# Kernel tuning notes

Measured on AMD Instinct MI355X. Metric: run time of the kernel, lower is better.

The kernel has to match this reference:

```python
import jax, jax.numpy as jnp
import numpy as np

B, T, D = 1, 4096, 1024
H = 16
HEAD_DIM = D // H
WINDOW = 256


def setup_inputs() -> dict:
    key = jax.random.key(0)
    k1, k2, k3 = jax.random.split(key, 3)
    x = jax.random.normal(k1, (B, T, D), dtype=jnp.float32)
    # torch nn.Linear(D, 3D) weight is (3D, D); we store transposed (D, 3D) for x @ W
    w_qkv = jax.random.normal(k2, (D, 3 * D), dtype=jnp.float32) * (1.0 / np.sqrt(D))
    w_out = jax.random.normal(k3, (D, D), dtype=jnp.float32) * (1.0 / np.sqrt(D))
    return {"x": x, "w_qkv": w_qkv, "w_out": w_out}


def reference(x, w_qkv, w_out):
    b, t, d = x.shape
    qkv = x @ w_qkv                                   # (B, T, 3D)
    q, k, v = jnp.split(qkv, 3, axis=-1)
    def split_heads(a):                               # (B, T, D) -> (B, H, T, dh)
        return a.reshape(b, t, H, HEAD_DIM).transpose(0, 2, 1, 3)
    q, k, v = split_heads(q), split_heads(k), split_heads(v)
    scale = jnp.sqrt(jnp.float32(HEAD_DIM))
    scores = jnp.einsum('bhqd,bhkd->bhqk', q, k) / scale   # (B, H, T, T)
    rows = jnp.arange(t)[:, None]
    cols = jnp.arange(t)[None, :]
    # causal sliding window: j <= i and j >= i - window + 1
    mask = (cols <= rows) & (cols >= rows - WINDOW + 1)     # (T, T) bool
    scores = jnp.where(mask[None, None], scores, -jnp.inf)
    attn = jax.nn.softmax(scores, axis=-1)
    out = jnp.einsum('bhqk,bhkd->bhqd', attn, v)            # (B, H, T, dh)
    out = out.transpose(0, 2, 1, 3).reshape(b, t, d)        # merge heads
    return out @ w_out
```

## Files before the change

### kernel.cpp

```cpp
#include <hip/hip_runtime.h>
#include <hip/hip_bf16.h>

#define T_SEQ 4096
#define DMODEL 1024
#define NH 16
#define DH 64
#define N_QKV 3072

typedef __attribute__((ext_vector_type(8))) short bf16x8;
typedef __attribute__((ext_vector_type(4))) float f32x4;

__device__ inline void gload_lds16(const __hip_bfloat16* g, __hip_bfloat16* l) {
  __builtin_amdgcn_global_load_lds(
      (const __attribute__((address_space(1))) void*)g,
      (__attribute__((address_space(3))) void*)l, 16, 0, 0);
}

__global__ void cast_x_kernel(const float* __restrict__ in,
                              __hip_bfloat16* __restrict__ out, int n) {
  int i = (blockIdx.x * 256 + threadIdx.x) * 4;
  if (i >= n) return;
  float4 v = *(const float4*)(in + i);
  ushort4 o;
  o.x = __bfloat16_as_ushort(__float2bfloat16(v.x));
  o.y = __bfloat16_as_ushort(__float2bfloat16(v.y));
  o.z = __bfloat16_as_ushort(__float2bfloat16(v.z));
  o.w = __bfloat16_as_ushort(__float2bfloat16(v.w));
  *(ushort4*)((unsigned short*)out + i) = o;
}

__global__ void transpose_cast_kernel(const float* __restrict__ in,
                                      __hip_bfloat16* __restrict__ out,
                                      int NN, int KK) {
  __shared__ float tile[32][33];
  int bn = blockIdx.x * 32, bk = blockIdx.y * 32;
  int tx = threadIdx.x & 31, ty = threadIdx.x >> 5;
#pragma unroll
  for (int r = 0; r < 32; r += 8)
    tile[ty + r][tx] = in[(size_t)(bk + ty + r) * NN + bn + tx];
  __syncthreads();
#pragma unroll
  for (int r = 0; r < 32; r += 8)
    out[(size_t)(bn + ty + r) * KK + bk + tx] = __float2bfloat16(tile[tx][ty + r]);
}

__global__ void transpose_v_kernel(const __hip_bfloat16* __restrict__ qkv,
                                   __hip_bfloat16* __restrict__ vt) {
  __shared__ unsigned short tile[32][33];
  int c0 = blockIdx.x * 32;
  int t0 = blockIdx.y * 32;
  int tx = threadIdx.x & 31, ty = threadIdx.x >> 5;
  const unsigned short* in = (const unsigned short*)qkv;
  unsigned short* out = (unsigned short*)vt;
#pragma unroll
  for (int r = 0; r < 32; r += 8)
    tile[ty + r][tx] = in[(size_t)(t0 + ty + r) * N_QKV + 2 * DMODEL + c0 + tx];
  __syncthreads();
#pragma unroll
  for (int r = 0; r < 32; r += 8)
    out[(size_t)(c0 + ty + r) * T_SEQ + t0 + tx] = tile[tx][ty + r];
}

__global__ __launch_bounds__(512, 2) void gemm8_qkv(
    const __hip_bfloat16* __restrict__ A, const __hip_bfloat16* __restrict__ Bt,
    __hip_bfloat16* __restrict__ C) {
  const int K = DMODEL;
  const int N = N_QKV;
  __shared__ alignas(16) __hip_bfloat16 Ab[3][256 * 64];
  __shared__ alignas(16) __hip_bfloat16 Bb[2][192 * 64];

  const int tid = threadIdx.x;
  const int lane = tid & 63;
  const int w = tid >> 6;
  const int wr = w >> 2, wc = w & 3;
  const int frow = lane & 15, fgrp = lane >> 4;

  const int bid = blockIdx.x;
  const int sbid = (bid & 7) * 32 + (bid >> 3);
  const int mb = sbid >> 4, nb = sbid & 15;
  const int brow = mb << 8, bcol = nb * 192;

  const int srow = lane >> 3;
  const int sslot = (lane & 7) ^ srow;
  const __hip_bfloat16* aSrcA = A + (size_t)(brow + w * 32 + srow) * K + sslot * 8;
  const __hip_bfloat16* aSrcB = Bt + (size_t)(bcol + w * 24 + srow) * K + sslot * 8;
  const int dstA = (w * 32 + srow) * 64 + (lane & 7) * 8;
  const int dstB = (w * 24 + srow) * 64 + (lane & 7) * 8;

  f32x4 acc[8][3] = {};

#pragma unroll
  for (int i = 0; i < 4; i++)
    gload_lds16(aSrcA + (size_t)(i * 8) * K, &Ab[0][dstA + i * 8 * 64]);
#pragma unroll
  for (int i = 0; i < 3; i++)
    gload_lds16(aSrcB + (size_t)(i * 8) * K, &Bb[0][dstB + i * 8 * 64]);
#pragma unroll
  for (int i = 0; i < 4; i++)
    gload_lds16(aSrcA + (size_t)(i * 8) * K + 64, &Ab[1][dstA + i * 8 * 64]);

  for (int t = 0; t < 16; ++t) {
    if (t < 15)
      asm volatile("s_waitcnt vmcnt(4)" ::: "memory");
    else
      asm volatile("s_waitcnt vmcnt(0)" ::: "memory");
    __builtin_amdgcn_s_barrier();

    const __hip_bfloat16* As = &Ab[t % 3][0];
    const __hip_bfloat16* Bs = &Bb[t & 1][0];
    bf16x8 bfrag[3][2], afrag[4][2];

#pragma unroll
    for (int n = 0; n < 3; n++) {
      int row = wc * 48 + n * 16 + frow;
#pragma unroll
      for (int kh = 0; kh < 2; kh++) {
        int slot = (kh * 4 + fgrp) ^ (row & 7);
        bfrag[n][kh] = *(const bf16x8*)(Bs + row * 64 + slot * 8);
      }
    }
#pragma unroll
    for (int m = 0; m < 4; m++) {
      int row = wr * 128 + m * 16 + frow;
#pragma unroll
      for (int kh = 0; kh < 2; kh++) {
        int slot = (kh * 4 + fgrp) ^ (row & 7);
        afrag[m][kh] = *(const bf16x8*)(As + row * 64 + slot * 8);
      }
    }
    if (t + 1 < 16) {
      __hip_bfloat16* bd = &Bb[(t + 1) & 1][0];
#pragma unroll
      for (int i = 0; i < 3; i++)
        gload_lds16(aSrcB + (size_t)(i * 8) * K + (t + 1) * 64, bd + dstB + i * 8 * 64);
    }
    __builtin_amdgcn_s_barrier();
    __builtin_amdgcn_s_setprio(1);
#pragma unroll
    for (int m = 0; m < 4; m++)
#pragma unroll
      for (int n = 0; n < 3; n++) {
        acc[m][n] = __builtin_amdgcn_mfma_f32_16x16x32_bf16(afrag[m][0], bfrag[n][0], acc[m][n], 0, 0, 0);
        acc[m][n] = __builtin_amdgcn_mfma_f32_16x16x32_bf16(afrag[m][1], bfrag[n][1], acc[m][n], 0, 0, 0);
      }
    __builtin_amdgcn_s_setprio(0);
    __builtin_amdgcn_s_barrier();

#pragma unroll
    for (int m = 0; m < 4; m++) {
      int row = wr * 128 + (m + 4) * 16 + frow;
#pragma unroll
      for (int kh = 0; kh < 2; kh++) {
        int slot = (kh * 4 + fgrp) ^ (row & 7);
        afrag[m][kh] = *(const bf16x8*)(As + row * 64 + slot * 8);
      }
    }
    if (t + 2 < 16) {
      __hip_bfloat16* ad = &Ab[(t + 2) % 3][0];
#pragma unroll
      for (int i = 0; i < 4; i++)
        gload_lds16(aSrcA + (size_t)(i * 8) * K + (t + 2) * 64, ad + dstA + i * 8 * 64);
    }
    __builtin_amdgcn_s_barrier();
    __builtin_amdgcn_s_setprio(1);
#pragma unroll
    for (int m = 0; m < 4; m++)
#pragma unroll
      for (int n = 0; n < 3; n++) {
        acc[m + 4][n] = __builtin_amdgcn_mfma_f32_16x16x32_bf16(afrag[m][0], bfrag[n][0], acc[m + 4][n], 0, 0, 0);
        acc[m + 4][n] = __builtin_amdgcn_mfma_f32_16x16x32_bf16(afrag[m][1], bfrag[n][1], acc[m + 4][n], 0, 0, 0);
      }
    __builtin_amdgcn_s_setprio(0);
  }

  const int orow0 = brow + wr * 128 + 4 * fgrp;
  const int ocol0 = bcol + wc * 48 + frow;
#pragma unroll
  for (int m = 0; m < 8; m++)
#pragma unroll
    for (int n = 0; n < 3; n++) {
      int col = ocol0 + n * 16;
      float sc = (col < DMODEL) ? 0.125f : 1.0f;
#pragma unroll
      for (int j = 0; j < 4; j++) {
        int row = orow0 + m * 16 + j;
        C[(size_t)row * N + col] = __float2bfloat16(acc[m][n][j] * sc);
      }
    }
}

__global__ __launch_bounds__(256) void gemm_out(
    const __hip_bfloat16* __restrict__ A, const __hip_bfloat16* __restrict__ Bt,
    float* __restrict__ C) {
  const int K = DMODEL, N = DMODEL;
  __shared__ alignas(16) __hip_bfloat16 Ab[4][128 * 32];
  __shared__ alignas(16) __hip_bfloat16 Bb[4][64 * 32];
  const int tid = threadIdx.x, lane = tid & 63, w = tid >> 6;
  const int wr = w >> 1, wc = w & 1;
  const int frow = lane & 15, fgrp = lane >> 4;
  const int bid = blockIdx.x;
  const int sbid = (bid & 7) * 64 + (bid >> 3);
  const int mb = sbid >> 4, nb = sbid & 15;
  const int brow = mb * 128, bcol = nb * 64;

  const int rrA = w * 32 + (lane >> 2);
  const int swzA = ((lane & 3) ^ ((rrA >> 1) & 3)) << 3;
  const int rrB = w * 16 + (lane >> 2);
  const int swzB = ((lane & 3) ^ ((rrB >> 1) & 3)) << 3;
  const __hip_bfloat16* aA0 = A + (size_t)(brow + rrA) * K + swzA;
  const __hip_bfloat16* aB0 = Bt + (size_t)(bcol + rrB) * K + swzB;
  const int dA0 = (w * 32) * 32, dA1 = (w * 32 + 16) * 32, dB0 = (w * 16) * 32;

  f32x4 acc[4][2] = {};
#pragma unroll
  for (int t = 0; t < 3; t++) {
    gload_lds16(aA0 + t * 32, &Ab[t][dA0]);
    gload_lds16(aA0 + 16 * (size_t)K + t * 32, &Ab[t][dA1]);
    gload_lds16(aB0 + t * 32, &Bb[t][dB0]);
  }
  for (int g = 0; g < 32; ++g) {
    if (g <= 29)
      asm volatile("s_waitcnt vmcnt(6)" ::: "memory");
    else if (g == 30)
      asm volatile("s_waitcnt vmcnt(3)" ::: "memory");
    else
      asm volatile("s_waitcnt vmcnt(0)" ::: "memory");
    __builtin_amdgcn_s_barrier();
    const __hip_bfloat16* As = Ab[g & 3];
    const __hip_bfloat16* Bs = Bb[g & 3];
    bf16x8 af[4], bfr[2];
#pragma unroll
    for (int m = 0; m < 4; m++) {
      int row = wr * 64 + m * 16 + frow;
      af[m] = *(const bf16x8*)(As + row * 32 + ((fgrp ^ ((row >> 1) & 3)) << 3));
    }
#pragma unroll
    for (int n = 0; n < 2; n++) {
      int row = wc * 32 + n * 16 + frow;
      bfr[n] = *(const bf16x8*)(Bs + row * 32 + ((fgrp ^ ((row >> 1) & 3)) << 3));
    }
    if (g <= 28) {
      int t = g + 3;
      gload_lds16(aA0 + t * 32, &Ab[t & 3][dA0]);
      gload_lds16(aA0 + 16 * (size_t)K + t * 32, &Ab[t & 3][dA1]);
      gload_lds16(aB0 + t * 32, &Bb[t & 3][dB0]);
    }
    __builtin_amdgcn_s_barrier();
    __builtin_amdgcn_s_setprio(1);
#pragma unroll
    for (int m = 0; m < 4; m++)
#pragma unroll
      for (int n = 0; n < 2; n++)
        acc[m][n] = __builtin_amdgcn_mfma_f32_16x16x32_bf16(af[m], bfr[n], acc[m][n], 0, 0, 0);
    __builtin_amdgcn_s_setprio(0);
  }
  const int orow0 = brow + wr * 64 + 4 * fgrp;
  const int ocol0 = bcol + wc * 32 + frow;
#pragma unroll
  for (int m = 0; m < 4; m++)
#pragma unroll
    for (int n = 0; n < 2; n++)
#pragma unroll
      for (int j = 0; j < 4; j++)
        C[(size_t)(orow0 + m * 16 + j) * N + ocol0 + n * 16] = acc[m][n][j];
}

__global__ __launch_bounds__(256) void swa_kernel(
    const __hip_bfloat16* __restrict__ qkv, const __hip_bfloat16* __restrict__ vt,
    __hip_bfloat16* __restrict__ attn_out) {
  const int b = blockIdx.x;
  const int s = (b & 7) * 128 + (b >> 3);
  const int h = s >> 6;
  const int qb = s & 63;
  const int tid = threadIdx.x;
  const int lane = tid & 63;
  const int w = tid >> 6;
  const int frow = lane & 15;
  const int fgrp = lane >> 4;
  const int fk = fgrp * 8;

  __shared__ alignas(16) __hip_bfloat16 Ks[2][64 * 64];
  __shared__ alignas(16) __hip_bfloat16 Vs[2][64 * 64];
  __shared__ alignas(16) __hip_bfloat16 Pl[4][16 * 72];

  const int qrow_g = qb * 64 + w * 16 + frow;
  bf16x8 aq[2];
  {
    const __hip_bfloat16* qptr = qkv + (size_t)qrow_g * N_QKV + h * DH;
    aq[0] = *(const bf16x8*)(qptr + fk);
    aq[1] = *(const bf16x8*)(qptr + 32 + fk);
  }

  f32x4 o[4] = {};
  float l_run[4] = {0.f, 0.f, 0.f, 0.f};

  const int srow = lane >> 3;
  const int ssw = (((lane & 7) ^ srow) << 3);
  const __hip_bfloat16* kbase =
      qkv + (size_t)(w * 16 + srow) * N_QKV + DMODEL + h * DH + ssw;
  const __hip_bfloat16* vbase =
      vt + (size_t)(h * DH + w * 16 + srow) * T_SEQ + ssw;

  const int kb0 = qb >= 4 ? qb - 4 : 0;

  {
    const __hip_bfloat16* ks = kbase + (size_t)kb0 * 64 * N_QKV;
    gload_lds16(ks, &Ks[0][w * 16 * 64]);
    gload_lds16(ks + 8 * (size_t)N_QKV, &Ks[0][(w * 16 + 8) * 64]);
    const __hip_bfloat16* vs = vbase + kb0 * 64;
    gload_lds16(vs, &Vs[0][w * 16 * 64]);
    gload_lds16(vs + 8 * (size_t)T_SEQ, &Vs[0][(w * 16 + 8) * 64]);
  }

  for (int kb = kb0; kb <= qb; kb++) {
    const int buf = (kb - kb0) & 1;
    if (kb < qb) {
      const __hip_bfloat16* ks = kbase + (size_t)(kb + 1) * 64 * N_QKV;
      gload_lds16(ks, &Ks[buf ^ 1][w * 16 * 64]);
      gload_lds16(ks + 8 * (size_t)N_QKV, &Ks[buf ^ 1][(w * 16 + 8) * 64]);
      const __hip_bfloat16* vs = vbase + (kb + 1) * 64;
      gload_lds16(vs, &Vs[buf ^ 1][w * 16 * 64]);
      gload_lds16(vs + 8 * (size_t)T_SEQ, &Vs[buf ^ 1][(w * 16 + 8) * 64]);
      asm volatile("s_waitcnt vmcnt(4)" ::: "memory");
    } else {
      asm volatile("s_waitcnt vmcnt(0)" ::: "memory");
    }
    __builtin_amdgcn_s_barrier();

    f32x4 sc[4];
#pragma unroll
    for (int n = 0; n < 4; n++) sc[n] = (f32x4){0.f, 0.f, 0.f, 0.f};
#pragma unroll
    for (int n = 0; n < 4; n++) {
      int rowk = n * 16 + frow;
      int x = rowk & 7;
      bf16x8 bk0 = *(const bf16x8*)(&Ks[buf][rowk * 64 + ((fgrp ^ x) << 3)]);
      bf16x8 bk1 = *(const bf16x8*)(&Ks[buf][rowk * 64 + (((4 + fgrp) ^ x) << 3)]);
      sc[n] = __builtin_amdgcn_mfma_f32_16x16x32_bf16(aq[0], bk0, sc[n], 0, 0, 0);
      sc[n] = __builtin_amdgcn_mfma_f32_16x16x32_bf16(aq[1], bk1, sc[n], 0, 0, 0);
    }

    const bool edge_hi = (kb == qb);
    const bool edge_lo = (kb == qb - 4);
#pragma unroll
    for (int r = 0; r < 4; r++) {
      const int row_l = w * 16 + 4 * fgrp + r;
      float rs = 0.f;
#pragma unroll
      for (int n = 0; n < 4; n++) {
        int col_l = n * 16 + frow;
        bool valid = (!edge_hi || col_l <= row_l) && (!edge_lo || col_l > row_l);
        float p = valid ? __expf(sc[n][r]) : 0.f;
        sc[n][r] = p;
        rs += p;
      }
      l_run[r] += rs;
    }

    __hip_bfloat16* pw = &Pl[w][0];
#pragma unroll
    for (int n = 0; n < 4; n++)
#pragma unroll
      for (int r = 0; r < 4; r++)
        pw[(4 * fgrp + r) * 72 + n * 16 + frow] = __float2bfloat16(sc[n][r]);

#pragma unroll
    for (int c = 0; c < 2; c++) {
      bf16x8 ap = *(const bf16x8*)(pw + frow * 72 + c * 32 + fk);
#pragma unroll
      for (int nd = 0; nd < 4; nd++) {
        int rowd = nd * 16 + frow;
        int x = rowd & 7;
        bf16x8 bv = *(const bf16x8*)(&Vs[buf][rowd * 64 + (((c * 4 + fgrp) ^ x) << 3)]);
        o[nd] = __builtin_amdgcn_mfma_f32_16x16x32_bf16(ap, bv, o[nd], 0, 0, 0);
      }
    }
    __builtin_amdgcn_s_barrier();
  }

#pragma unroll
  for (int r = 0; r < 4; r++) {
    float l = l_run[r];
    l += __shfl_xor(l, 1);
    l += __shfl_xor(l, 2);
    l += __shfl_xor(l, 4);
    l += __shfl_xor(l, 8);
    l_run[r] = l;
  }
#pragma unroll
  for (int nd = 0; nd < 4; nd++)
#pragma unroll
    for (int r = 0; r < 4; r++) {
      float v = o[nd][r] / l_run[r];
      attn_out[(size_t)(qb * 64 + w * 16 + 4 * fgrp + r) * DMODEL + h * DH + nd * 16 + frow] =
          __float2bfloat16(v);
    }
}

extern "C" void kernel_launch(void* const* d_in, const int* in_sizes, int n_in,
                              void* d_out, int out_size, void* d_ws, size_t ws_size,
                              hipStream_t stream) {
  const float* x = (const float*)d_in[0];
  const float* w_qkv = (const float*)d_in[1];
  const float* w_out = (const float*)d_in[2];
  float* out = (float*)d_out;

  char* ws = (char*)d_ws;
  __hip_bfloat16* x_bf = (__hip_bfloat16*)ws;
  __hip_bfloat16* vt = (__hip_bfloat16*)ws;
  __hip_bfloat16* wqkvT = (__hip_bfloat16*)(ws + 8388608);
  __hip_bfloat16* woutT = (__hip_bfloat16*)(ws + 14680064);
  __hip_bfloat16* qkv_bf = (__hip_bfloat16*)(ws + 16777216);
  __hip_bfloat16* attn_bf = (__hip_bfloat16*)(ws + 41943040);

  cast_x_kernel<<<4096, 256, 0, stream>>>(x, x_bf, T_SEQ * DMODEL);
  transpose_cast_kernel<<<dim3(N_QKV / 32, DMODEL / 32), 256, 0, stream>>>(w_qkv, wqkvT, N_QKV, DMODEL);
  transpose_cast_kernel<<<dim3(DMODEL / 32, DMODEL / 32), 256, 0, stream>>>(w_out, woutT, DMODEL, DMODEL);

  gemm8_qkv<<<(T_SEQ / 256) * (N_QKV / 192), 512, 0, stream>>>(x_bf, wqkvT, qkv_bf);

  transpose_v_kernel<<<dim3(DMODEL / 32, T_SEQ / 32), 256, 0, stream>>>(qkv_bf, vt);

  swa_kernel<<<(T_SEQ / 64) * NH, 256, 0, stream>>>(qkv_bf, vt, attn_bf);

  gemm_out<<<512, 256, 0, stream>>>(attn_bf, woutT, out);
}
```

Baseline: 85.82 us.

## Fuse prep kernels, split QKV GEMM k-halves, enlarge output GEMM tile

Folds the x cast and both weight transpose-casts into one launch indexed by block id, removing two kernel launches. Restructures the QKV GEMM inner loop into four phases, one per 32-wide k half and A half, with smaller fragment sets and the next tile's global-to-LDS loads split across the phases. This is meant to cut register pressure and spread memory traffic. The output GEMM moves from 128x64 to 128x128 tiles with half the blocks, for more operand reuse at the cost of fewer blocks in flight and more LDS per block.

```diff
diff --git a/kernel.cpp b/kernel.cpp
--- a/kernel.cpp
+++ b/kernel.cpp
@@ -16,24 +16,37 @@
       (__attribute__((address_space(3))) void*)l, 16, 0, 0);
 }
 
-__global__ void cast_x_kernel(const float* __restrict__ in,
-                              __hip_bfloat16* __restrict__ out, int n) {
-  int i = (blockIdx.x * 256 + threadIdx.x) * 4;
-  if (i >= n) return;
-  float4 v = *(const float4*)(in + i);
-  ushort4 o;
-  o.x = __bfloat16_as_ushort(__float2bfloat16(v.x));
-  o.y = __bfloat16_as_ushort(__float2bfloat16(v.y));
-  o.z = __bfloat16_as_ushort(__float2bfloat16(v.z));
-  o.w = __bfloat16_as_ushort(__float2bfloat16(v.w));
-  *(ushort4*)((unsigned short*)out + i) = o;
-}
-
-__global__ void transpose_cast_kernel(const float* __restrict__ in,
-                                      __hip_bfloat16* __restrict__ out,
-                                      int NN, int KK) {
+__global__ void prep_kernel(const float* __restrict__ x,
+                            const float* __restrict__ w_qkv,
+                            const float* __restrict__ w_out,
+                            __hip_bfloat16* __restrict__ x_bf,
+                            __hip_bfloat16* __restrict__ wqkvT,
+                            __hip_bfloat16* __restrict__ woutT) {
   __shared__ float tile[32][33];
-  int bn = blockIdx.x * 32, bk = blockIdx.y * 32;
+  const int b = blockIdx.x;
+  if (b < 4096) {
+    int i = (b * 256 + threadIdx.x) * 4;
+    float4 v = *(const float4*)(x + i);
+    ushort4 o;
+    o.x = __bfloat16_as_ushort(__float2bfloat16(v.x));
+    o.y = __bfloat16_as_ushort(__float2bfloat16(v.y));
+    o.z = __bfloat16_as_ushort(__float2bfloat16(v.z));
+    o.w = __bfloat16_as_ushort(__float2bfloat16(v.w));
+    *(ushort4*)((unsigned short*)x_bf + i) = o;
+    return;
+  }
+  const float* in;
+  __hip_bfloat16* out;
+  int NN, KK, bn, bk;
+  if (b < 7168) {
+    int idx = b - 4096;
+    in = w_qkv; out = wqkvT; NN = N_QKV; KK = DMODEL;
+    bn = (idx % 96) * 32; bk = (idx / 96) * 32;
+  } else {
+    int idx = b - 7168;
+    in = w_out; out = woutT; NN = DMODEL; KK = DMODEL;
+    bn = (idx % 32) * 32; bk = (idx / 32) * 32;
+  }
   int tx = threadIdx.x & 31, ty = threadIdx.x >> 5;
 #pragma unroll
   for (int r = 0; r < 32; r += 8)
@@ -108,68 +121,93 @@
 
     const __hip_bfloat16* As = &Ab[t % 3][0];
     const __hip_bfloat16* Bs = &Bb[t & 1][0];
-    bf16x8 bfrag[3][2], afrag[4][2];
-
+    bf16x8 bfrag[3], af[4];
+
+    if (t + 1 < 16) {
+      __hip_bfloat16* bd = &Bb[(t + 1) & 1][0];
+#pragma unroll
+      for (int i = 0; i < 3; i++)
+        gload_lds16(aSrcB + (size_t)(i * 8) * K + (t + 1) * 64, bd + dstB + i * 8 * 64);
+    }
 #pragma unroll
     for (int n = 0; n < 3; n++) {
       int row = wc * 48 + n * 16 + frow;
-#pragma unroll
-      for (int kh = 0; kh < 2; kh++) {
-        int slot = (kh * 4 + fgrp) ^ (row & 7);
-        bfrag[n][kh] = *(const bf16x8*)(Bs + row * 64 + slot * 8);
-      }
+      bfrag[n] = *(const bf16x8*)(Bs + row * 64 + (fgrp ^ (row & 7)) * 8);
     }
 #pragma unroll
     for (int m = 0; m < 4; m++) {
       int row = wr * 128 + m * 16 + frow;
-#pragma unroll
-      for (int kh = 0; kh < 2; kh++) {
-        int slot = (kh * 4 + fgrp) ^ (row & 7);
-        afrag[m][kh] = *(const bf16x8*)(As + row * 64 + slot * 8);
-      }
-    }
-    if (t + 1 < 16) {
-      __hip_bfloat16* bd = &Bb[(t + 1) & 1][0];
-#pragma unroll
-      for (int i = 0; i < 3; i++)
-        gload_lds16(aSrcB + (size_t)(i * 8) * K + (t + 1) * 64, bd + dstB + i * 8 * 64);
+      af[m] = *(const bf16x8*)(As + row * 64 + (fgrp ^ (row & 7)) * 8);
     }
     __builtin_amdgcn_s_barrier();
     __builtin_amdgcn_s_setprio(1);
 #pragma unroll
     for (int m = 0; m < 4; m++)
 #pragma unroll
-      for (int n = 0; n < 3; n++) {
-        acc[m][n] = __builtin_amdgcn_mfma_f32_16x16x32_bf16(afrag[m][0], bfrag[n][0], acc[m][n], 0, 0, 0);
-        acc[m][n] = __builtin_amdgcn_mfma_f32_16x16x32_bf16(afrag[m][1], bfrag[n][1], acc[m][n], 0, 0, 0);
-      }
+      for (int n = 0; n < 3; n++)
+        acc[m][n] = __builtin_amdgcn_mfma_f32_16x16x32_bf16(af[m], bfrag[n], acc[m][n], 0, 0, 0);
     __builtin_amdgcn_s_setprio(0);
     __builtin_amdgcn_s_barrier();
 
+    if (t + 2 < 16) {
+      __hip_bfloat16* ad = &Ab[(t + 2) % 3][0];
+#pragma unroll
+      for (int i = 0; i < 2; i++)
+        gload_lds16(aSrcA + (size_t)(i * 8) * K + (t + 2) * 64, ad + dstA + i * 8 * 64);
+    }
 #pragma unroll
     for (int m = 0; m < 4; m++) {
       int row = wr * 128 + (m + 4) * 16 + frow;
-#pragma unroll
-      for (int kh = 0; kh < 2; kh++) {
-        int slot = (kh * 4 + fgrp) ^ (row & 7);
-        afrag[m][kh] = *(const bf16x8*)(As + row * 64 + slot * 8);
-      }
-    }
+      af[m] = *(const bf16x8*)(As + row * 64 + (fgrp ^ (row & 7)) * 8);
+    }
+    __builtin_amdgcn_s_barrier();
+    __builtin_amdgcn_s_setprio(1);
+#pragma unroll
+    for (int m = 0; m < 4; m++)
+#pragma unroll
+      for (int n = 0; n < 3; n++)
+        acc[m + 4][n] = __builtin_amdgcn_mfma_f32_16x16x32_bf16(af[m], bfrag[n], acc[m + 4][n], 0, 0, 0);
+    __builtin_amdgcn_s_setprio(0);
+    __builtin_amdgcn_s_barrier();
+
     if (t + 2 < 16) {
       __hip_bfloat16* ad = &Ab[(t + 2) % 3][0];
 #pragma unroll
-      for (int i = 0; i < 4; i++)
+      for (int i = 2; i < 4; i++)
         gload_lds16(aSrcA + (size_t)(i * 8) * K + (t + 2) * 64, ad + dstA + i * 8 * 64);
     }
+#pragma unroll
+    for (int n = 0; n < 3; n++) {
+      int row = wc * 48 + n * 16 + frow;
+      bfrag[n] = *(const bf16x8*)(Bs + row * 64 + ((4 + fgrp) ^ (row & 7)) * 8);
+    }
+#pragma unroll
+    for (int m = 0; m < 4; m++) {
+      int row = wr * 128 + m * 16 + frow;
+      af[m] = *(const bf16x8*)(As + row * 64 + ((4 + fgrp) ^ (row & 7)) * 8);
+    }
     __builtin_amdgcn_s_barrier();
     __builtin_amdgcn_s_setprio(1);
 #pragma unroll
     for (int m = 0; m < 4; m++)
 #pragma unroll
-      for (int n = 0; n < 3; n++) {
-        acc[m + 4][n] = __builtin_amdgcn_mfma_f32_16x16x32_bf16(afrag[m][0], bfrag[n][0], acc[m + 4][n], 0, 0, 0);
-        acc[m + 4][n] = __builtin_amdgcn_mfma_f32_16x16x32_bf16(afrag[m][1], bfrag[n][1], acc[m + 4][n], 0, 0, 0);
-      }
+      for (int n = 0; n < 3; n++)
+        acc[m][n] = __builtin_amdgcn_mfma_f32_16x16x32_bf16(af[m], bfrag[n], acc[m][n], 0, 0, 0);
+    __builtin_amdgcn_s_setprio(0);
+    __builtin_amdgcn_s_barrier();
+
+#pragma unroll
+    for (int m = 0; m < 4; m++) {
+      int row = wr * 128 + (m + 4) * 16 + frow;
+      af[m] = *(const bf16x8*)(As + row * 64 + ((4 + fgrp) ^ (row & 7)) * 8);
+    }
+    __builtin_amdgcn_s_barrier();
+    __builtin_amdgcn_s_setprio(1);
+#pragma unroll
+    for (int m = 0; m < 4; m++)
+#pragma unroll
+      for (int n = 0; n < 3; n++)
+        acc[m + 4][n] = __builtin_amdgcn_mfma_f32_16x16x32_bf16(af[m], bfrag[n], acc[m + 4][n], 0, 0, 0);
     __builtin_amdgcn_s_setprio(0);
   }
 
@@ -194,72 +232,72 @@
     float* __restrict__ C) {
   const int K = DMODEL, N = DMODEL;
   __shared__ alignas(16) __hip_bfloat16 Ab[4][128 * 32];
-  __shared__ alignas(16) __hip_bfloat16 Bb[4][64 * 32];
+  __shared__ alignas(16) __hip_bfloat16 Bb[4][128 * 32];
   const int tid = threadIdx.x, lane = tid & 63, w = tid >> 6;
   const int wr = w >> 1, wc = w & 1;
   const int frow = lane & 15, fgrp = lane >> 4;
   const int bid = blockIdx.x;
-  const int sbid = (bid & 7) * 64 + (bid >> 3);
-  const int mb = sbid >> 4, nb = sbid & 15;
-  const int brow = mb * 128, bcol = nb * 64;
-
-  const int rrA = w * 32 + (lane >> 2);
-  const int swzA = ((lane & 3) ^ ((rrA >> 1) & 3)) << 3;
-  const int rrB = w * 16 + (lane >> 2);
-  const int swzB = ((lane & 3) ^ ((rrB >> 1) & 3)) << 3;
-  const __hip_bfloat16* aA0 = A + (size_t)(brow + rrA) * K + swzA;
-  const __hip_bfloat16* aB0 = Bt + (size_t)(bcol + rrB) * K + swzB;
-  const int dA0 = (w * 32) * 32, dA1 = (w * 32 + 16) * 32, dB0 = (w * 16) * 32;
-
-  f32x4 acc[4][2] = {};
+  const int sbid = (bid & 7) * 32 + (bid >> 3);
+  const int mb = sbid >> 3, nb = sbid & 7;
+  const int brow = mb * 128, bcol = nb * 128;
+
+  const int sr = tid >> 2;
+  const int swz = ((tid & 3) ^ ((sr >> 1) & 3)) << 3;
+  const __hip_bfloat16* aA = A + (size_t)(brow + sr) * K + swz;
+  const __hip_bfloat16* aB = Bt + (size_t)(bcol + sr) * K + swz;
+  const int dlo = sr * 32 + (tid & 3) * 8;
+  const int dhi = (sr + 64) * 32 + (tid & 3) * 8;
+
+  f32x4 acc[4][4] = {};
 #pragma unroll
   for (int t = 0; t < 3; t++) {
-    gload_lds16(aA0 + t * 32, &Ab[t][dA0]);
-    gload_lds16(aA0 + 16 * (size_t)K + t * 32, &Ab[t][dA1]);
-    gload_lds16(aB0 + t * 32, &Bb[t][dB0]);
-  }
-  for (int g = 0; g < 32; ++g) {
-    if (g <= 29)
-      asm volatile("s_waitcnt vmcnt(6)" ::: "memory");
-    else if (g == 30)
-      asm volatile("s_waitcnt vmcnt(3)" ::: "memory");
+    gload_lds16(aA + t * 32, &Ab[t][dlo]);
+    gload_lds16(aA + 64 * (size_t)K + t * 32, &Ab[t][dhi]);
+    gload_lds16(aB + t * 32, &Bb[t][dlo]);
+    gload_lds16(aB + 64 * (size_t)K + t * 32, &Bb[t][dhi]);
+  }
+  for (int t = 0; t < 32; ++t) {
+    if (t < 30)
+      asm volatile("s_waitcnt vmcnt(8)" ::: "memory");
+    else if (t == 30)
+      asm volatile("s_waitcnt vmcnt(4)" ::: "memory");
     else
       asm volatile("s_waitcnt vmcnt(0)" ::: "memory");
     __builtin_amdgcn_s_barrier();
-    const __hip_bfloat16* As = Ab[g & 3];
-    const __hip_bfloat16* Bs = Bb[g & 3];
-    bf16x8 af[4], bfr[2];
+    const __hip_bfloat16* As = Ab[t & 3];
+    const __hip_bfloat16* Bs = Bb[t & 3];
+    if (t + 3 < 32) {
+      gload_lds16(aA + (t + 3) * 32, &Ab[(t + 3) & 3][dlo]);
+      gload_lds16(aA + 64 * (size_t)K + (t + 3) * 32, &Ab[(t + 3) & 3][dhi]);
+      gload_lds16(aB + (t + 3) * 32, &Bb[(t + 3) & 3][dlo]);
+      gload_lds16(aB + 64 * (size_t)K + (t + 3) * 32, &Bb[(t + 3) & 3][dhi]);
+    }
+    bf16x8 af[4], bfr[4];
 #pragma unroll
     for (int m = 0; m < 4; m++) {
       int row = wr * 64 + m * 16 + frow;
       af[m] = *(const bf16x8*)(As + row * 32 + ((fgrp ^ ((row >> 1) & 3)) << 3));
     }
 #pragma unroll
-    for (int n = 0; n < 2; n++) {
-      int row = wc * 32 + n * 16 + frow;
+    for (int n = 0; n < 4; n++) {
+      int row = wc * 64 + n * 16 + frow;
       bfr[n] = *(const bf16x8*)(Bs + row * 32 + ((fgrp ^ ((row >> 1) & 3)) << 3));
     }
-    if (g <= 28) {
-      int t = g + 3;
-      gload_lds16(aA0 + t * 32, &Ab[t & 3][dA0]);
-      gload_lds16(aA0 + 16 * (size_t)K + t * 32, &Ab[t & 3][dA1]);
-      gload_lds16(aB0 + t * 32, &Bb[t & 3][dB0]);
-    }
     __builtin_amdgcn_s_barrier();
     __builtin_amdgcn_s_setprio(1);
 #pragma unroll
     for (int m = 0; m < 4; m++)
 #pragma unroll
-      for (int n = 0; n < 2; n++)
+      for (int n = 0; n < 4; n++)
         acc[m][n] = __builtin_amdgcn_mfma_f32_16x16x32_bf16(af[m], bfr[n], acc[m][n], 0, 0, 0);
     __builtin_amdgcn_s_setprio(0);
   }
   const int orow0 = brow + wr * 64 + 4 * fgrp;
-  const int ocol0 = bcol + wc * 32 + frow;
+  const int ocol0 = bcol + wc * 64 + frow;
 #pragma unroll
   for (int m = 0; m < 4; m++)
 #pragma unroll
-    for (int n = 0; n < 2; n++)
+    for (int n = 0; n < 4; n++)
 #pragma unroll
       for (int j = 0; j < 4; j++)
         C[(size_t)(orow0 + m * 16 + j) * N + ocol0 + n * 16] = acc[m][n][j];
@@ -413,9 +451,7 @@
   __hip_bfloat16* qkv_bf = (__hip_bfloat16*)(ws + 16777216);
   __hip_bfloat16* attn_bf = (__hip_bfloat16*)(ws + 41943040);
 
-  cast_x_kernel<<<4096, 256, 0, stream>>>(x, x_bf, T_SEQ * DMODEL);
-  transpose_cast_kernel<<<dim3(N_QKV / 32, DMODEL / 32), 256, 0, stream>>>(w_qkv, wqkvT, N_QKV, DMODEL);
-  transpose_cast_kernel<<<dim3(DMODEL / 32, DMODEL / 32), 256, 0, stream>>>(w_out, woutT, DMODEL, DMODEL);
+  prep_kernel<<<8192, 256, 0, stream>>>(x, w_qkv, w_out, x_bf, wqkvT, woutT);
 
   gemm8_qkv<<<(T_SEQ / 256) * (N_QKV / 192), 512, 0, stream>>>(x_bf, wqkvT, qkv_bf);
 
@@ -423,5 +459,5 @@
 
   swa_kernel<<<(T_SEQ / 64) * NH, 256, 0, stream>>>(qkv_bf, vt, attn_bf);
 
-  gemm_out<<<512, 256, 0, stream>>>(attn_bf, woutT, out);
-}
+  gemm_out<<<256, 256, 0, stream>>>(attn_bf, woutT, out);
+}
```

Measured after the change: 102.2 us. +19.1%, slower.
